# Optimization experiments

Hardware: AMD Instinct MI355X
Metric: run time of the kernel (lower is better)

## Reference

```python
import jax, jax.numpy as jnp
import numpy as np

UP = 2
KSIZE = 3
RES = 64
LRELU_SLOPE = 0.2
ACT_GAIN = float(np.sqrt(2.0))  # def_gain of 'lrelu' in bias_act


def _setup_filter():
    # upfirdn2d.setup_filter([1,3,3,1]): normalize, make separable 2D filter
    f = jnp.array([1.0, 3.0, 3.0, 1.0], dtype=jnp.float32)
    f = f / jnp.sum(f)
    return jnp.outer(f, f)  # [4,4]


def _upfirdn2d_up2(x, f2):
    # Zero-insertion upsample by 2 + pad + FIR filter, gain = up**2.
    # Torch path: zero-insert to 2H, pad (3,2), conv 4-tap -> 2H+2.
    # lhs_dilation gives 2H-1; absorbing the trailing inserted zero into the
    # right pad ((3,3) instead of (3,2)) is exactly equivalent.
    B, C, H, W = x.shape
    k = (f2 * (UP * UP)).astype(x.dtype)[None, None]  # [1,1,4,4] (symmetric, flip-invariant)
    k = jnp.tile(k, (C, 1, 1, 1))                     # depthwise [C,1,4,4]
    return jax.lax.conv_general_dilated(
        x, k, window_strides=(1, 1), padding=((3, 3), (3, 3)),
        lhs_dilation=(UP, UP),
        dimension_numbers=('NCHW', 'OIHW', 'NCHW'),
        feature_group_count=C)


def setup_inputs() -> dict:
    key = jax.random.key(0)
    ks = jax.random.split(key, 6)
    B, Cin, Cout, Wd = 16, 512, 512, 512
    Hin = RES // UP
    return {
        "x": jax.random.normal(ks[0], (B, Cin, Hin, Hin), jnp.float32),
        "w": jax.random.normal(ks[1], (B, Wd), jnp.float32),
        "affine_weight": jax.random.normal(ks[2], (Cin, Wd), jnp.float32),
        "affine_bias": jnp.ones((Cin,), jnp.float32),  # bias_init=1
        "weight": jax.random.normal(ks[3], (Cout, Cin, KSIZE, KSIZE), jnp.float32),
        "bias": jnp.zeros((Cout,), jnp.float32),
        "noise_const": jax.random.normal(ks[4], (RES, RES), jnp.float32),
        "noise_strength": jax.random.uniform(ks[5], (), jnp.float32),
    }


def reference(x, w, affine_weight, affine_bias, weight, bias, noise_const, noise_strength):
    B, Cin, Hin, Win = x.shape
    Cout = weight.shape[0]
    # affine: FullyConnectedLayer, weight_gain = 1/sqrt(w_dim), bias_init=1
    styles = w @ affine_weight.T * (1.0 / np.sqrt(w.shape[1])) + affine_bias  # [B,Cin]
    # modulate + demodulate (fused_modconv=True): per-sample weights
    wmod = weight[None] * styles[:, None, :, None, None]                     # [B,Cout,Cin,kh,kw]
    dcoef = jax.lax.rsqrt(jnp.sum(jnp.square(wmod), axis=(2, 3, 4)) + 1e-8)  # [B,Cout]
    wmod = wmod * dcoef[:, :, None, None, None]
    # up=2 -> flip_weight=False -> true convolution: flip spatial taps
    wmod = wmod[..., ::-1, ::-1]
    # conv2d_resample: upfirdn2d upsample first (pad = k//2 + (fw+up-1)//2 = 3), then VALID conv
    xu = _upfirdn2d_up2(x, _setup_filter())                                  # [B,Cin,66,66]
    xr = xu.reshape(1, B * Cin, xu.shape[2], xu.shape[3])
    wr = wmod.reshape(B * Cout, Cin, KSIZE, KSIZE)
    y = jax.lax.conv_general_dilated(
        xr, wr, window_strides=(1, 1), padding='VALID',
        dimension_numbers=('NCHW', 'OIHW', 'NCHW'),
        feature_group_count=B)
    y = y.reshape(B, Cout, RES, RES)
    # noise_mode='const': noise = noise_const * noise_strength
    y = y + noise_const * noise_strength
    # fused bias + lrelu + def_gain (gain=1, conv_clamp=None)
    y = jax.nn.leaky_relu(y + bias[None, :, None, None], LRELU_SLOPE) * ACT_GAIN
    return y
```

## Files before the change

### kernel.cpp

```cpp
#include <hip/hip_runtime.h>
#include <hip/hip_bf16.h>
#include <math.h>

#define CIN   512
#define COUT  512
#define NB    16
#define WD    512
#define HIN   32
#define HUP   66
#define RES   64
#define LRELU 0.2f
#define ACT_GAIN 1.4142135623730951f

typedef __attribute__((ext_vector_type(8))) short short8;
typedef __attribute__((ext_vector_type(4))) float float4v;

__global__ void styles2_kernel(const float* __restrict__ w,
                               const float* __restrict__ aw,
                               const float* __restrict__ ab,
                               float* __restrict__ styles) {
    int b = blockIdx.x;
    int cig = blockIdx.y;
    int lane = threadIdx.x & 63, wv = threadIdx.x >> 6;
    __shared__ float wsh[WD];
    for (int e = threadIdx.x; e < WD; e += 256) wsh[e] = w[b * WD + e];
    __syncthreads();
    for (int r = 0; r < 16; ++r) {
        int ci = cig * 64 + wv * 16 + r;
        const float* arow = aw + (size_t)ci * WD;
        float acc = 0.f;
        for (int k = lane; k < WD; k += 64) acc += arow[k] * wsh[k];
        for (int off = 32; off; off >>= 1) acc += __shfl_down(acc, off, 64);
        if (lane == 0)
            styles[b * CIN + ci] = acc * 0.04419417382415922f + ab[ci];
    }
}

__global__ void prep_weights(const float* __restrict__ weight,
                             float* __restrict__ wsq,
                             __hip_bfloat16* __restrict__ wb) {
    int idx = blockIdx.x * 256 + threadIdx.x;
    int co = idx & (COUT - 1);
    int ci = idx >> 9;
    const float* wp = weight + ((size_t)co * CIN + ci) * 9;
    int cc = ci >> 5, chi = (ci >> 3) & 3, clo = ci & 7;
    float s = 0.f;
#pragma unroll
    for (int t = 0; t < 9; ++t) {
        float v = wp[t];
        s += v * v;
        int tf = 8 - t;
        wb[((((size_t)cc * 9 + tf) * 4 + chi) * COUT + co) * 8 + clo] = __float2bfloat16(v);
    }
    wsq[(size_t)co * CIN + ci] = s;
}

__global__ void dcoef2_kernel(const float* __restrict__ styles,
                              const float* __restrict__ wsq,
                              float* __restrict__ dcoef) {
    int b = blockIdx.x;
    int cog = blockIdx.y;
    int lane = threadIdx.x & 63, wv = threadIdx.x >> 6;
    __shared__ float s2[CIN];
    for (int e = threadIdx.x; e < CIN; e += 256) {
        float s = styles[b * CIN + e];
        s2[e] = s * s;
    }
    __syncthreads();
    for (int r = 0; r < 16; ++r) {
        int co = cog * 64 + wv * 16 + r;
        const float* qrow = wsq + (size_t)co * CIN;
        float acc = 0.f;
        for (int k = lane; k < CIN; k += 64) acc += qrow[k] * s2[k];
        for (int off = 32; off; off >>= 1) acc += __shfl_down(acc, off, 64);
        if (lane == 0) dcoef[b * COUT + co] = rsqrtf(acc + 1e-8f);
    }
}

__global__ void upmod2_kernel(const float* __restrict__ x,
                              const float* __restrict__ styles,
                              __hip_bfloat16* __restrict__ xs2) {
    __shared__ float xt[128 * 68];
    __shared__ float ssh[128];
    const int oh = blockIdx.x;
    const int ci0 = blockIdx.y * 128;
    const int b = blockIdx.z;
    int m0, m1; float a0, a1;
    if (oh & 1) { m0 = (oh - 3) >> 1; a0 = 0.125f; m1 = (oh - 1) >> 1; a1 = 0.375f; }
    else        { m0 = (oh >> 1) - 1; a0 = 0.375f; m1 = (oh >> 1);     a1 = 0.125f; }
    if (threadIdx.x < 128) ssh[threadIdx.x] = styles[b * CIN + ci0 + threadIdx.x] * 4.0f;
    for (int e = threadIdx.x; e < 2048; e += 256) {
        int ci = e >> 4, sel = (e >> 3) & 1, iw4 = e & 7;
        int m = sel ? m1 : m0;
        float4v v = (float4v)0.f;
        if (m >= 0 && m < HIN)
            v = *(const float4v*)(x + ((size_t)(b * CIN + ci0 + ci) * HIN + m) * HIN + iw4 * 4);
        *(float4v*)(&xt[ci * 68 + sel * 32 + iw4 * 4]) = v;
    }
    __syncthreads();
    for (int e = threadIdx.x; e < 1056; e += 256) {
        int cig = e / 66;
        int ow = e - cig * 66;
        int n0i, n1i; float b0, b1;
        if (ow & 1) { n0i = (ow - 3) >> 1; b0 = 0.125f; n1i = (ow - 1) >> 1; b1 = 0.375f; }
        else        { n0i = (ow >> 1) - 1; b0 = 0.375f; n1i = (ow >> 1);     b1 = 0.125f; }
        bool c0 = (n0i >= 0) & (n0i < HIN);
        bool c1 = (n1i >= 0) & (n1i < HIN);
        short8 sv;
#pragma unroll
        for (int u = 0; u < 8; ++u) {
            int ci = cig * 8 + u;
            const float* base = &xt[ci * 68];
            float r0 = (c0 ? base[n0i] : 0.f) * b0 + (c1 ? base[n1i] : 0.f) * b1;
            float r1 = (c0 ? base[32 + n0i] : 0.f) * b0 + (c1 ? base[32 + n1i] : 0.f) * b1;
            float val = (a0 * r0 + a1 * r1) * ssh[ci];
            __hip_bfloat16 h = __float2bfloat16(val);
            sv[u] = *reinterpret_cast<const short*>(&h);
        }
        *reinterpret_cast<short8*>(
            xs2 + (((size_t)b * HUP + oh) * HUP + ow) * CIN + ci0 + cig * 8) = sv;
    }
}

#define LDA_SZ 43008
#define LDB_SZ 38016
#define LDS_TOT (LDA_SZ + LDB_SZ)

__global__ __launch_bounds__(256, 2) void conv_mfma(
        const __hip_bfloat16* __restrict__ xs2,
        const __hip_bfloat16* __restrict__ wb,
        const float* __restrict__ dcoef,
        const float* __restrict__ bias,
        const float* __restrict__ noise,
        const float* __restrict__ nstr,
        float* __restrict__ out)
{
    extern __shared__ __align__(16) char smem[];
    const int tid = threadIdx.x;
    const int lane = tid & 63;
    const int wid = tid >> 6;
    const int li = lane & 15;
    const int q = lane >> 4;
    const int mb = blockIdx.x;
    const int n0 = blockIdx.y * 64;
    const int b  = blockIdx.z;
    const int y0 = mb * 8;

    int a_goff[11];
    int a_lds[11];
#pragma unroll
    for (int k = 0; k < 11; ++k) {
        int n = wid + k * 4;
        if (n < 42) {
            int s = n * 64 + lane;
            if (s > 2639) s = 2639;
            int r = s / 264;
            int rem = s - r * 264;
            int chi = rem / 66;
            int col = rem - chi * 66;
            a_goff[k] = ((b * HUP + y0 + r) * HUP + col) * CIN + chi * 8;
            a_lds[k] = n * 1024;
        } else { a_goff[k] = 0; a_lds[k] = -1; }
    }
    int b_goff[9], b_lds[9];
#pragma unroll
    for (int k = 0; k < 9; ++k) {
        int sl = wid + k * 4;
        b_goff[k] = (sl * COUT + n0 + lane) * 8;
        b_lds[k] = LDA_SZ + (sl >> 2) * 4224 + (sl & 3) * 1056;
    }

    float4v acc[8][4];
#pragma unroll
    for (int i = 0; i < 8; ++i)
#pragma unroll
        for (int j = 0; j < 4; ++j) acc[i][j] = (float4v)0.f;

    const char* xg = (const char*)xs2;
    const char* wg = (const char*)wb;

    for (int cc = 0; cc < 16; ++cc) {
#pragma unroll
        for (int k = 0; k < 9; ++k) {
            long ge = (long)(b_goff[k] + cc * 147456);
            __builtin_amdgcn_global_load_lds(
                (const __attribute__((address_space(1))) char*)(wg + ge * 2),
                (__attribute__((address_space(3))) char*)(smem + b_lds[k]),
                16, 0, 0);
        }
#pragma unroll
        for (int k = 0; k < 11; ++k) {
            if (a_lds[k] >= 0) {
                long ge = (long)(a_goff[k] + cc * 32);
                __builtin_amdgcn_global_load_lds(
                    (const __attribute__((address_space(1))) char*)(xg + ge * 2),
                    (__attribute__((address_space(3))) char*)(smem + a_lds[k]),
                    16, 0, 0);
            }
        }
        __syncthreads();

#pragma unroll
        for (int t = 0; t < 9; ++t) {
            const int kh = t / 3, kw = t - kh * 3;
            short8 bf[4];
#pragma unroll
            for (int j = 0; j < 4; ++j)
                bf[j] = *(const short8*)(smem + LDA_SZ + t * 4224 + q * 1056 +
                                         (j * 16 + li) * 16);
#pragma unroll
            for (int i = 0; i < 8; ++i) {
                int rl = wid * 2 + (i >> 2) + kh;
                short8 af = *(const short8*)(smem +
                        ((rl * 4 + q) * 66 + ((i & 3) * 16 + li + kw)) * 16);
#pragma unroll
                for (int j = 0; j < 4; ++j)
                    acc[i][j] = __builtin_amdgcn_mfma_f32_16x16x32_bf16(
                        af, bf[j], acc[i][j], 0, 0, 0);
            }
        }
        __syncthreads();
    }

    const float ns = nstr[0];
#pragma unroll
    for (int j = 0; j < 4; ++j) {
        int cout = n0 + j * 16 + li;
        float dc = dcoef[b * COUT + cout];
        float bs = bias[cout];
#pragma unroll
        for (int i = 0; i < 8; ++i) {
            int row = y0 + wid * 2 + (i >> 2);
            int colb = (i & 3) * 16 + q * 4;
            float* op = out + ((size_t)(b * COUT + cout) * RES + row) * RES + colb;
            float4v nz = *(const float4v*)(noise + row * RES + colb);
            float4v a = acc[i][j];
            float4v r;
            r.x = a.x * dc + nz.x * ns + bs;
            r.y = a.y * dc + nz.y * ns + bs;
            r.z = a.z * dc + nz.z * ns + bs;
            r.w = a.w * dc + nz.w * ns + bs;
            r.x = (r.x > 0.f ? r.x : LRELU * r.x) * ACT_GAIN;
            r.y = (r.y > 0.f ? r.y : LRELU * r.y) * ACT_GAIN;
            r.z = (r.z > 0.f ? r.z : LRELU * r.z) * ACT_GAIN;
            r.w = (r.w > 0.f ? r.w : LRELU * r.w) * ACT_GAIN;
            *(float4v*)op = r;
        }
    }
}

extern "C" void kernel_launch(void* const* d_in, const int* in_sizes, int n_in,
                              void* d_out, int out_size, void* d_ws, size_t ws_size,
                              hipStream_t stream) {
    (void)in_sizes; (void)n_in; (void)out_size; (void)ws_size;
    const float* x     = (const float*)d_in[0];
    const float* w     = (const float*)d_in[1];
    const float* aw    = (const float*)d_in[2];
    const float* ab    = (const float*)d_in[3];
    const float* wt    = (const float*)d_in[4];
    const float* bias  = (const float*)d_in[5];
    const float* noise = (const float*)d_in[6];
    const float* nstr  = (const float*)d_in[7];
    float* out = (float*)d_out;

    static bool init = false;
    if (!init) {
        hipFuncSetAttribute(reinterpret_cast<const void*>(conv_mfma),
                            hipFuncAttributeMaxDynamicSharedMemorySize, LDS_TOT);
        init = true;
    }

    char* ws = (char*)d_ws;
    float* styles = (float*)ws;
    float* dcoef  = (float*)(ws + 32768);
    float* wsq    = (float*)(ws + 65536);
    __hip_bfloat16* wb  = (__hip_bfloat16*)(ws + 65536 + 1048576);
    __hip_bfloat16* xs2 = (__hip_bfloat16*)(ws + 65536 + 1048576 + 4718592);

    styles2_kernel<<<dim3(NB, 8), dim3(256), 0, stream>>>(w, aw, ab, styles);
    prep_weights<<<dim3(1024), dim3(256), 0, stream>>>(wt, wsq, wb);
    dcoef2_kernel<<<dim3(NB, 8), dim3(256), 0, stream>>>(styles, wsq, dcoef);
    upmod2_kernel<<<dim3(HUP, 4, NB), dim3(256), 0, stream>>>(x, styles, xs2);
    conv_mfma<<<dim3(8, 8, NB), dim3(256), LDS_TOT, stream>>>(
        xs2, wb, dcoef, bias, noise, nstr, out);
}
```

Baseline: 523.9 us.

## Double-buffer conv LDS tiles with 512-thread blocks and prefetch overlap

The conv kernel moves to 512 threads per block, so each of 8 waves computes one output row instead of two, and it double-buffers the A and B tiles in LDS. The next channel chunk is prefetched with global_load_lds while MFMAs run on the current buffer, and s_setprio raises priority during compute. The B layout is simplified by dropping padding. The goal is to hide global-load latency behind compute, at the cost of doubling LDS to about 160KB, which limits occupancy to one block per CU, and fewer MFMAs per wave per LDS read.

```diff
diff --git a/kernel.cpp b/kernel.cpp
--- a/kernel.cpp
+++ b/kernel.cpp
@@ -122,11 +122,12 @@
     }
 }
 
-#define LDA_SZ 43008
-#define LDB_SZ 38016
-#define LDS_TOT (LDA_SZ + LDB_SZ)
-
-__global__ __launch_bounds__(256, 2) void conv_mfma(
+#define ABUF 43008
+#define BBUF 36864
+#define BUFSZ (ABUF + BBUF)
+#define LDS_TOT (2 * BUFSZ)
+
+__global__ __launch_bounds__(512, 1) void conv_mfma(
         const __hip_bfloat16* __restrict__ xs2,
         const __hip_bfloat16* __restrict__ wb,
         const float* __restrict__ dcoef,
@@ -146,93 +147,115 @@
     const int b  = blockIdx.z;
     const int y0 = mb * 8;
 
-    int a_goff[11];
-    int a_lds[11];
-#pragma unroll
-    for (int k = 0; k < 11; ++k) {
-        int n = wid + k * 4;
-        if (n < 42) {
-            int s = n * 64 + lane;
-            if (s > 2639) s = 2639;
-            int r = s / 264;
-            int rem = s - r * 264;
-            int chi = rem / 66;
-            int col = rem - chi * 66;
-            a_goff[k] = ((b * HUP + y0 + r) * HUP + col) * CIN + chi * 8;
-            a_lds[k] = n * 1024;
-        } else { a_goff[k] = 0; a_lds[k] = -1; }
-    }
-    int b_goff[9], b_lds[9];
-#pragma unroll
-    for (int k = 0; k < 9; ++k) {
-        int sl = wid + k * 4;
+    int a_goff[6];
+#pragma unroll
+    for (int k = 0; k < 6; ++k) {
+        int n = wid + k * 8;
+        int s = n * 64 + lane;
+        if (s > 2639) s = 2639;
+        int r = s / 264;
+        int rem = s - r * 264;
+        int chi = rem / 66;
+        int col = rem - chi * 66;
+        a_goff[k] = ((b * HUP + y0 + r) * HUP + col) * CIN + chi * 8;
+    }
+    int b_goff[5];
+#pragma unroll
+    for (int k = 0; k < 5; ++k) {
+        int sl = wid + k * 8;
         b_goff[k] = (sl * COUT + n0 + lane) * 8;
-        b_lds[k] = LDA_SZ + (sl >> 2) * 4224 + (sl & 3) * 1056;
-    }
-
-    float4v acc[8][4];
-#pragma unroll
-    for (int i = 0; i < 8; ++i)
+    }
+
+    float4v acc[4][4];
+#pragma unroll
+    for (int i = 0; i < 4; ++i)
 #pragma unroll
         for (int j = 0; j < 4; ++j) acc[i][j] = (float4v)0.f;
 
     const char* xg = (const char*)xs2;
     const char* wg = (const char*)wb;
 
-    for (int cc = 0; cc < 16; ++cc) {
-#pragma unroll
-        for (int k = 0; k < 9; ++k) {
-            long ge = (long)(b_goff[k] + cc * 147456);
-            __builtin_amdgcn_global_load_lds(
-                (const __attribute__((address_space(1))) char*)(wg + ge * 2),
-                (__attribute__((address_space(3))) char*)(smem + b_lds[k]),
-                16, 0, 0);
-        }
-#pragma unroll
-        for (int k = 0; k < 11; ++k) {
-            if (a_lds[k] >= 0) {
-                long ge = (long)(a_goff[k] + cc * 32);
-                __builtin_amdgcn_global_load_lds(
-                    (const __attribute__((address_space(1))) char*)(xg + ge * 2),
-                    (__attribute__((address_space(3))) char*)(smem + a_lds[k]),
-                    16, 0, 0);
-            }
-        }
-        __syncthreads();
-
-#pragma unroll
-        for (int t = 0; t < 9; ++t) {
-            const int kh = t / 3, kw = t - kh * 3;
-            short8 bf[4];
-#pragma unroll
-            for (int j = 0; j < 4; ++j)
-                bf[j] = *(const short8*)(smem + LDA_SZ + t * 4224 + q * 1056 +
-                                         (j * 16 + li) * 16);
-#pragma unroll
-            for (int i = 0; i < 8; ++i) {
-                int rl = wid * 2 + (i >> 2) + kh;
-                short8 af = *(const short8*)(smem +
-                        ((rl * 4 + q) * 66 + ((i & 3) * 16 + li + kw)) * 16);
-#pragma unroll
-                for (int j = 0; j < 4; ++j)
-                    acc[i][j] = __builtin_amdgcn_mfma_f32_16x16x32_bf16(
-                        af, bf[j], acc[i][j], 0, 0, 0);
-            }
-        }
-        __syncthreads();
-    }
+#define STAGE(CC, BUFB) do {                                                  \
+        _Pragma("unroll")                                                     \
+        for (int k = 0; k < 5; ++k) {                                         \
+            int sl = wid + k * 8;                                             \
+            if (sl < 36) {                                                    \
+                long ge = (long)(b_goff[k] + (CC) * 147456);                  \
+                __builtin_amdgcn_global_load_lds(                             \
+                    (const __attribute__((address_space(1))) char*)(wg + ge * 2), \
+                    (__attribute__((address_space(3))) char*)(smem + (BUFB) + ABUF + sl * 1024), \
+                    16, 0, 0);                                                \
+            }                                                                 \
+        }                                                                     \
+        _Pragma("unroll")                                                     \
+        for (int k = 0; k < 6; ++k) {                                         \
+            int n = wid + k * 8;                                              \
+            if (n < 42) {                                                     \
+                long ge = (long)(a_goff[k] + (CC) * 32);                      \
+                __builtin_amdgcn_global_load_lds(                             \
+                    (const __attribute__((address_space(1))) char*)(xg + ge * 2), \
+                    (__attribute__((address_space(3))) char*)(smem + (BUFB) + n * 1024), \
+                    16, 0, 0);                                                \
+            }                                                                 \
+        }                                                                     \
+    } while (0)
+
+#define COMPUTE(BUFB) do {                                                    \
+        __builtin_amdgcn_s_setprio(1);                                        \
+        _Pragma("unroll")                                                     \
+        for (int t = 0; t < 9; ++t) {                                         \
+            const int kh = t / 3, kw = t - kh * 3;                            \
+            short8 bf[4];                                                     \
+            _Pragma("unroll")                                                 \
+            for (int j = 0; j < 4; ++j)                                       \
+                bf[j] = *(const short8*)(smem + (BUFB) + ABUF +               \
+                        (((t * 4 + q) * 64) + j * 16 + li) * 16);             \
+            _Pragma("unroll")                                                 \
+            for (int i = 0; i < 4; ++i) {                                     \
+                short8 af = *(const short8*)(smem + (BUFB) +                  \
+                        ((((wid + kh) * 4 + q) * 66) + (i * 16 + li + kw)) * 16); \
+                _Pragma("unroll")                                             \
+                for (int j = 0; j < 4; ++j)                                   \
+                    acc[i][j] = __builtin_amdgcn_mfma_f32_16x16x32_bf16(      \
+                        af, bf[j], acc[i][j], 0, 0, 0);                       \
+            }                                                                 \
+        }                                                                     \
+        __builtin_amdgcn_s_setprio(0);                                        \
+    } while (0)
+
+#define SYNC() do {                                                           \
+        asm volatile("s_waitcnt vmcnt(0)" ::: "memory");                      \
+        __builtin_amdgcn_s_barrier();                                         \
+    } while (0)
+
+    STAGE(0, 0);
+    SYNC();
+
+#pragma unroll 1
+    for (int cc = 0; cc < 16; cc += 2) {
+        STAGE(cc + 1, BUFSZ);
+        COMPUTE(0);
+        SYNC();
+        if (cc + 2 < 16) STAGE(cc + 2, 0);
+        COMPUTE(BUFSZ);
+        SYNC();
+    }
+
+#undef STAGE
+#undef COMPUTE
+#undef SYNC
 
     const float ns = nstr[0];
+    const int row = y0 + wid;
 #pragma unroll
     for (int j = 0; j < 4; ++j) {
         int cout = n0 + j * 16 + li;
         float dc = dcoef[b * COUT + cout];
         float bs = bias[cout];
-#pragma unroll
-        for (int i = 0; i < 8; ++i) {
-            int row = y0 + wid * 2 + (i >> 2);
-            int colb = (i & 3) * 16 + q * 4;
-            float* op = out + ((size_t)(b * COUT + cout) * RES + row) * RES + colb;
+        float* op = out + ((size_t)(b * COUT + cout) * RES + row) * RES;
+#pragma unroll
+        for (int i = 0; i < 4; ++i) {
+            int colb = i * 16 + q * 4;
             float4v nz = *(const float4v*)(noise + row * RES + colb);
             float4v a = acc[i][j];
             float4v r;
@@ -244,7 +267,7 @@
             r.y = (r.y > 0.f ? r.y : LRELU * r.y) * ACT_GAIN;
             r.z = (r.z > 0.f ? r.z : LRELU * r.z) * ACT_GAIN;
             r.w = (r.w > 0.f ? r.w : LRELU * r.w) * ACT_GAIN;
-            *(float4v*)op = r;
+            *(float4v*)(op + colb) = r;
         }
     }
 }
@@ -281,6 +304,6 @@
     prep_weights<<<dim3(1024), dim3(256), 0, stream>>>(wt, wsq, wb);
     dcoef2_kernel<<<dim3(NB, 8), dim3(256), 0, stream>>>(styles, wsq, dcoef);
     upmod2_kernel<<<dim3(HUP, 4, NB), dim3(256), 0, stream>>>(x, styles, xs2);
-    conv_mfma<<<dim3(8, 8, NB), dim3(256), LDS_TOT, stream>>>(
+    conv_mfma<<<dim3(8, 8, NB), dim3(512), LDS_TOT, stream>>>(
         xs2, wb, dcoef, bias, noise, nstr, out);
 }
```

After: 492.6 us. 1.06x faster.
